# Performance work log

Hardware: AMD Instinct MI355X
Metric: run time of the kernel (lower is better)

## Reference

```python
import jax, jax.numpy as jnp
import numpy as np

N = 50000      # nodes
E = 800000     # edges (before self-loops)
IN_C = 128
H_C = 64
HEADS = 4
OUT_C = 16
NEG_SLOPE = 0.2  # PyG GATConv default


def setup_inputs() -> dict:
    key = jax.random.key(0)
    ks = jax.random.split(key, 11)
    x = jax.random.normal(ks[0], (N, IN_C), dtype=jnp.float32)
    edge_index = jax.random.randint(ks[1], (2, E), 0, N, dtype=jnp.int64)
    def p(k, shape, fan_in):
        return jax.random.normal(k, shape, dtype=jnp.float32) / np.sqrt(fan_in)
    return {
        "x": x,
        "edge_index": edge_index,
        "W1": p(ks[2], (IN_C, HEADS * H_C), IN_C),
        "att_src1": p(ks[3], (HEADS, H_C), H_C),
        "att_dst1": p(ks[4], (HEADS, H_C), H_C),
        "b1": jnp.zeros((HEADS * H_C,), dtype=jnp.float32),
        "W2": p(ks[5], (HEADS * H_C, OUT_C), HEADS * H_C),
        "att_src2": p(ks[6], (1, OUT_C), OUT_C),
        "att_dst2": p(ks[7], (1, OUT_C), OUT_C),
        "b2": jnp.zeros((OUT_C,), dtype=jnp.float32),
    }


def _gat_layer(x, src, dst, W, a_src, a_dst, b, concat):
    n = x.shape[0]
    heads, C = a_src.shape
    h = (x @ W).reshape(n, heads, C)                      # [N,H,C]
    al_s = jnp.einsum('nhc,hc->nh', h, a_src)             # [N,H]
    al_d = jnp.einsum('nhc,hc->nh', h, a_dst)
    e = jax.nn.leaky_relu(al_s[src] + al_d[dst], NEG_SLOPE)  # [E,H]
    # segment softmax over destination neighborhoods
    m = jax.lax.stop_gradient(jax.ops.segment_max(e, dst, num_segments=n))
    p = jnp.exp(e - m[dst])
    denom = jax.ops.segment_sum(p, dst, num_segments=n)
    alpha = p / (denom[dst] + 1e-16)                      # [E,H]
    out = jax.ops.segment_sum(alpha[:, :, None] * h[src], dst, num_segments=n)  # [N,H,C]
    out = out.reshape(n, heads * C) if concat else out.mean(axis=1)
    return out + b


def reference(x, edge_index, W1, att_src1, att_dst1, b1, W2, att_src2, att_dst2, b2):
    # PyG GATConv add_self_loops=True
    loop = jnp.arange(N, dtype=edge_index.dtype)
    src = jnp.concatenate([edge_index[0], loop])
    dst = jnp.concatenate([edge_index[1], loop])
    h = jax.nn.relu(_gat_layer(x, src, dst, W1, att_src1, att_dst1, b1, True))
    out = _gat_layer(h, src, dst, W2, att_src2, att_dst2, b2, False)
    return jax.nn.log_softmax(out, axis=-1)
```

## Files before the change

kernel.cpp:

```cpp
#include <hip/hip_runtime.h>
#include <hip/hip_fp16.h>
#include <cstdint>
#include <cstddef>

#define NEG 0.2f

typedef _Float16 f16x8 __attribute__((ext_vector_type(8)));
typedef float f32x4 __attribute__((ext_vector_type(4)));

__device__ inline float lrelu(float v) { return v > 0.f ? v : NEG * v; }

__global__ void k_swzW(const float* __restrict__ W1, f16x8* __restrict__ W1s) {
  int tau = blockIdx.x * 256 + threadIdx.x;
  if (tau >= 4096) return;
  int l = tau & 63, ct = (tau >> 6) & 15, ks = tau >> 10;
  int col = ct * 16 + (l & 15);
  f16x8 v;
  #pragma unroll
  for (int j = 0; j < 8; j++) {
    int k = ks * 32 + ((j < 4) ? ((l >> 4) * 4 + j) : (16 + (l >> 4) * 4 + (j - 4)));
    v[j] = (_Float16)W1[k * 256 + col];
  }
  W1s[tau] = v;
}

__global__ __launch_bounds__(256) void k_gemm1f(const float* __restrict__ X,
                                                const f16x8* __restrict__ W1s,
                                                const float* __restrict__ as1,
                                                const float* __restrict__ ad1,
                                                __half* __restrict__ H16,
                                                float* __restrict__ als,
                                                float* __restrict__ ald, int N) {
  __shared__ __align__(16) char lds[32768];
  _Float16* A = (_Float16*)lds;
  int t = threadIdx.x;
  int rb = blockIdx.x * 64;
  int l = t & 63, wv = t >> 6;

  #pragma unroll
  for (int i = 0; i < 8; i++) {
    int idx = i * 256 + t;
    int row = idx >> 5, q = idx & 31;
    int gr = rb + row; if (gr >= N) gr = N - 1;
    float4 xv = *(const float4*)(X + (size_t)gr * 128 + q * 4);
    int ks = q >> 3, g = q & 3, hg = (q >> 2) & 1;
    int gran = (ks * 4 + g) ^ (row & 7);
    _Float16* dst = A + row * 128 + gran * 8 + hg * 4;
    dst[0] = (_Float16)xv.x; dst[1] = (_Float16)xv.y;
    dst[2] = (_Float16)xv.z; dst[3] = (_Float16)xv.w;
  }
  __syncthreads();

  f32x4 acc[4][4] = {};
  #pragma unroll
  for (int ks = 0; ks < 4; ks++) {
    f16x8 bfr[4];
    #pragma unroll
    for (int ct = 0; ct < 4; ct++)
      bfr[ct] = W1s[(ks * 16 + wv * 4 + ct) * 64 + l];
    #pragma unroll
    for (int rt = 0; rt < 4; rt++) {
      int row = rt * 16 + (l & 15);
      int gran = (ks * 4 + (l >> 4)) ^ (row & 7);
      f16x8 afr = *(const f16x8*)(A + row * 128 + gran * 8);
      #pragma unroll
      for (int ct = 0; ct < 4; ct++)
        acc[rt][ct] = __builtin_amdgcn_mfma_f32_16x16x32_f16(afr, bfr[ct], acc[rt][ct], 0, 0, 0);
    }
  }

  float asv[4], adv[4];
  #pragma unroll
  for (int ct = 0; ct < 4; ct++) {
    asv[ct] = as1[wv * 64 + ct * 16 + (l & 15)];
    adv[ct] = ad1[wv * 64 + ct * 16 + (l & 15)];
  }
  #pragma unroll
  for (int rt = 0; rt < 4; rt++) {
    #pragma unroll
    for (int j = 0; j < 4; j++) {
      float ps = 0.f, pd = 0.f;
      #pragma unroll
      for (int ct = 0; ct < 4; ct++) {
        ps += acc[rt][ct][j] * asv[ct];
        pd += acc[rt][ct][j] * adv[ct];
      }
      ps += __shfl_xor(ps, 1); ps += __shfl_xor(ps, 2);
      ps += __shfl_xor(ps, 4); ps += __shfl_xor(ps, 8);
      pd += __shfl_xor(pd, 1); pd += __shfl_xor(pd, 2);
      pd += __shfl_xor(pd, 4); pd += __shfl_xor(pd, 8);
      if ((l & 15) == 0) {
        int gr = rb + rt * 16 + (l >> 4) * 4 + j;
        if (gr < N) { als[gr * 4 + wv] = ps; ald[gr * 4 + wv] = pd; }
      }
    }
  }

  __syncthreads();
  _Float16* HL = (_Float16*)lds;
  #pragma unroll
  for (int rt = 0; rt < 4; rt++) {
    #pragma unroll
    for (int j = 0; j < 4; j++) {
      int row = rt * 16 + (l >> 4) * 4 + j;
      #pragma unroll
      for (int ct = 0; ct < 4; ct++) {
        int col = wv * 64 + ct * 16 + (l & 15);
        int g2 = (col >> 3) ^ ((row & 7) << 2);
        HL[row * 256 + g2 * 8 + (col & 7)] = (_Float16)acc[rt][ct][j];
      }
    }
  }
  __syncthreads();
  #pragma unroll
  for (int i = 0; i < 8; i++) {
    int idx = i * 256 + t;
    int row = idx >> 5, g = idx & 31;
    int g2 = g ^ ((row & 7) << 2);
    f32x4 v = *(const f32x4*)(HL + row * 256 + g2 * 8);
    int gr = rb + row;
    if (gr < N) *(f32x4*)((char*)H16 + (size_t)gr * 512 + g * 16) = v;
  }
}

__global__ void k_deg(const int* __restrict__ ei, int* __restrict__ deg, int E, int ET) {
  int e = blockIdx.x * 256 + threadIdx.x;
  if (e >= ET) return;
  int d = (e < E) ? ei[E + e] : e - E;
  atomicAdd(&deg[d], 1);
}

__global__ __launch_bounds__(256) void k_scan_partial(const int* __restrict__ deg,
                                                      int* __restrict__ bsum, int N) {
  __shared__ int sd[256];
  int t = threadIdx.x;
  int base = blockIdx.x * 1024 + t * 4;
  int s = 0;
  #pragma unroll
  for (int j = 0; j < 4; j++) { int i = base + j; s += (i < N) ? deg[i] : 0; }
  sd[t] = s;
  __syncthreads();
  for (int o = 128; o > 0; o >>= 1) {
    if (t < o) sd[t] += sd[t + o];
    __syncthreads();
  }
  if (t == 0) bsum[blockIdx.x] = sd[0];
}

__global__ void k_scan_sums(const int* __restrict__ bsum, int* __restrict__ boff,
                            int* __restrict__ offsets, int NB, int N) {
  if (threadIdx.x == 0 && blockIdx.x == 0) {
    int run = 0;
    for (int i = 0; i < NB; i++) { boff[i] = run; run += bsum[i]; }
    offsets[N] = run;
  }
}

__global__ __launch_bounds__(256) void k_scan_final(const int* __restrict__ deg,
                                                    const int* __restrict__ boff,
                                                    int* __restrict__ offsets,
                                                    int* __restrict__ cursor, int N) {
  __shared__ int sd[256];
  int t = threadIdx.x;
  int base = blockIdx.x * 1024 + t * 4;
  int v[4]; int s = 0;
  #pragma unroll
  for (int j = 0; j < 4; j++) { int i = base + j; v[j] = (i < N) ? deg[i] : 0; s += v[j]; }
  int my = s;
  sd[t] = s;
  __syncthreads();
  for (int o = 1; o < 256; o <<= 1) {
    int add = (t >= o) ? sd[t - o] : 0;
    __syncthreads();
    sd[t] += add;
    __syncthreads();
  }
  int run = sd[t] - my + boff[blockIdx.x];
  #pragma unroll
  for (int j = 0; j < 4; j++) {
    int i = base + j;
    if (i < N) { offsets[i] = run; cursor[i] = run; run += v[j]; }
  }
}

__global__ void k_fill(const int* __restrict__ ei, int* __restrict__ cursor,
                       const float* __restrict__ als, const float* __restrict__ ald,
                       int* __restrict__ csr_src, float* __restrict__ pw1,
                       int* __restrict__ pos_arr, int E, int ET) {
  int e = blockIdx.x * 256 + threadIdx.x;
  if (e >= ET) return;
  int s, d;
  if (e < E) { s = ei[e]; d = ei[E + e]; } else { s = d = e - E; }
  int pos = atomicAdd(&cursor[d], 1);
  csr_src[pos] = s;
  pos_arr[e] = pos;
  float4 a = *(const float4*)(als + (size_t)s * 4);
  float4 b = *(const float4*)(ald + (size_t)d * 4);
  float4 p;
  p.x = __expf(lrelu(a.x + b.x));
  p.y = __expf(lrelu(a.y + b.y));
  p.z = __expf(lrelu(a.z + b.z));
  p.w = __expf(lrelu(a.w + b.w));
  *(float4*)(pw1 + (size_t)pos * 4) = p;
}

__device__ inline void acc8(float4 v, float p, float* a, float& s) {
  __half2 h0 = __builtin_bit_cast(__half2, v.x);
  __half2 h1 = __builtin_bit_cast(__half2, v.y);
  __half2 h2 = __builtin_bit_cast(__half2, v.z);
  __half2 h3 = __builtin_bit_cast(__half2, v.w);
  float2 f0 = __half22float2(h0), f1 = __half22float2(h1);
  float2 f2 = __half22float2(h2), f3 = __half22float2(h3);
  a[0] += p * f0.x; a[1] += p * f0.y; a[2] += p * f1.x; a[3] += p * f1.y;
  a[4] += p * f2.x; a[5] += p * f2.y; a[6] += p * f3.x; a[7] += p * f3.y;
  s += p;
}

__global__ __launch_bounds__(256) void k_agg1(const int* __restrict__ off,
                                              const int* __restrict__ csr_src,
                                              const float* __restrict__ pw1,
                                              const float4* __restrict__ H16,
                                              const float* __restrict__ b1,
                                              __half* __restrict__ H2, int N) {
  int t = threadIdx.x;
  int n = blockIdx.x * 8 + (t >> 5);
  if (n >= N) return;
  int lane = t & 31;
  int g = lane >> 3;
  int st = off[n], en = off[n + 1];
  float a[8] = {0.f, 0.f, 0.f, 0.f, 0.f, 0.f, 0.f, 0.f};
  float s = 0.f;
  int i = st;
  for (; i + 4 <= en; i += 4) {
    int s0 = csr_src[i], s1 = csr_src[i + 1], s2 = csr_src[i + 2], s3 = csr_src[i + 3];
    float p0 = pw1[(size_t)i * 4 + g];
    float p1 = pw1[(size_t)(i + 1) * 4 + g];
    float p2 = pw1[(size_t)(i + 2) * 4 + g];
    float p3 = pw1[(size_t)(i + 3) * 4 + g];
    float4 v0 = H16[(size_t)s0 * 32 + lane];
    float4 v1 = H16[(size_t)s1 * 32 + lane];
    float4 v2 = H16[(size_t)s2 * 32 + lane];
    float4 v3 = H16[(size_t)s3 * 32 + lane];
    acc8(v0, p0, a, s); acc8(v1, p1, a, s); acc8(v2, p2, a, s); acc8(v3, p3, a, s);
  }
  for (; i < en; i++) {
    int s0 = csr_src[i];
    float p0 = pw1[(size_t)i * 4 + g];
    float4 v0 = H16[(size_t)s0 * 32 + lane];
    acc8(v0, p0, a, s);
  }
  float inv = 1.f / (s + 1e-16f);
  int c0 = lane * 8;
  float4 bb0 = *(const float4*)(b1 + c0);
  float4 bb1 = *(const float4*)(b1 + c0 + 4);
  f16x8 o;
  o[0] = (_Float16)fmaxf(a[0] * inv + bb0.x, 0.f);
  o[1] = (_Float16)fmaxf(a[1] * inv + bb0.y, 0.f);
  o[2] = (_Float16)fmaxf(a[2] * inv + bb0.z, 0.f);
  o[3] = (_Float16)fmaxf(a[3] * inv + bb0.w, 0.f);
  o[4] = (_Float16)fmaxf(a[4] * inv + bb1.x, 0.f);
  o[5] = (_Float16)fmaxf(a[5] * inv + bb1.y, 0.f);
  o[6] = (_Float16)fmaxf(a[6] * inv + bb1.z, 0.f);
  o[7] = (_Float16)fmaxf(a[7] * inv + bb1.w, 0.f);
  *(f16x8*)((char*)H2 + (size_t)n * 512 + lane * 16) = o;
}

__global__ __launch_bounds__(256) void k_gemm2(const __half* __restrict__ H2,
                                               const float* __restrict__ W2,
                                               const float* __restrict__ as2,
                                               const float* __restrict__ ad2,
                                               float* __restrict__ Z,
                                               float* __restrict__ als2,
                                               float* __restrict__ ald2, int N) {
  __shared__ float w2s[4096];
  int t = threadIdx.x;
  for (int i = t; i < 4096; i += 256) w2s[i] = W2[i];
  __syncthreads();
  int n = blockIdx.x * 16 + (t >> 4);
  int c = t & 15;
  if (n >= N) return;
  const f16x8* hp = (const f16x8*)((const char*)H2 + (size_t)n * 512);
  float acc = 0.f;
  #pragma unroll 8
  for (int kb = 0; kb < 32; kb++) {
    f16x8 hv = hp[kb];
    #pragma unroll
    for (int j = 0; j < 8; j++)
      acc += (float)hv[j] * w2s[(kb * 8 + j) * 16 + c];
  }
  Z[(size_t)n * 16 + c] = acc;
  float ps = acc * as2[c], pd = acc * ad2[c];
  #pragma unroll
  for (int o = 8; o > 0; o >>= 1) {
    ps += __shfl_down(ps, o, 16);
    pd += __shfl_down(pd, o, 16);
  }
  if (c == 0) { als2[n] = ps; ald2[n] = pd; }
}

__global__ void k_score2p(const int* __restrict__ ei, const int* __restrict__ pos_arr,
                          const float* __restrict__ als2, const float* __restrict__ ald2,
                          float* __restrict__ pw2, int E, int ET) {
  int e = blockIdx.x * 256 + threadIdx.x;
  if (e >= ET) return;
  int s, d;
  if (e < E) { s = ei[e]; d = ei[E + e]; } else { s = d = e - E; }
  float v = lrelu(als2[s] + ald2[d]);
  pw2[pos_arr[e]] = __expf(v);
}

__global__ __launch_bounds__(256) void k_agg2(const int* __restrict__ off,
                                              const int* __restrict__ csr_src,
                                              const float* __restrict__ pw2,
                                              const float* __restrict__ Z,
                                              const float* __restrict__ b2,
                                              float* __restrict__ out, int N) {
  int t = threadIdx.x;
  int n = blockIdx.x * 16 + (t >> 4);
  if (n >= N) return;
  int c = t & 15;
  int st = off[n], en = off[n + 1];
  float s = 0.f, acc = 0.f;
  int i = st;
  for (; i + 4 <= en; i += 4) {
    int s0 = csr_src[i], s1 = csr_src[i + 1], s2 = csr_src[i + 2], s3 = csr_src[i + 3];
    float p0 = pw2[i], p1 = pw2[i + 1], p2 = pw2[i + 2], p3 = pw2[i + 3];
    float z0 = Z[(size_t)s0 * 16 + c];
    float z1 = Z[(size_t)s1 * 16 + c];
    float z2 = Z[(size_t)s2 * 16 + c];
    float z3 = Z[(size_t)s3 * 16 + c];
    acc += p0 * z0 + p1 * z1 + p2 * z2 + p3 * z3;
    s += p0 + p1 + p2 + p3;
  }
  for (; i < en; i++) {
    int s0 = csr_src[i];
    float p0 = pw2[i];
    acc += p0 * Z[(size_t)s0 * 16 + c];
    s += p0;
  }
  float v = acc / (s + 1e-16f) + b2[c];
  float mx = v;
  #pragma unroll
  for (int o = 8; o > 0; o >>= 1) mx = fmaxf(mx, __shfl_xor(mx, o, 16));
  float ex = __expf(v - mx);
  float sm = ex;
  #pragma unroll
  for (int o = 8; o > 0; o >>= 1) sm += __shfl_xor(sm, o, 16);
  out[(size_t)n * 16 + c] = v - mx - logf(sm);
}

extern "C" void kernel_launch(void* const* d_in, const int* in_sizes, int n_in,
                              void* d_out, int out_size, void* d_ws, size_t ws_size,
                              hipStream_t stream) {
  const float* x   = (const float*)d_in[0];
  const int*   ei  = (const int*)d_in[1];
  const float* W1  = (const float*)d_in[2];
  const float* as1 = (const float*)d_in[3];
  const float* ad1 = (const float*)d_in[4];
  const float* b1  = (const float*)d_in[5];
  const float* W2  = (const float*)d_in[6];
  const float* as2 = (const float*)d_in[7];
  const float* ad2 = (const float*)d_in[8];
  const float* b2  = (const float*)d_in[9];
  float* out = (float*)d_out;

  int N  = in_sizes[0] / 128;
  int E  = in_sizes[1] / 2;
  int ET = E + N;
  int NB = (N + 1023) / 1024;

  char* w = (char*)d_ws;
  size_t off_b = 0;
  auto alloc = [&](size_t bytes) -> char* {
    size_t start = (off_b + 255) & ~(size_t)255;
    off_b = start + bytes;
    return w + start;
  };
  __half*   h16  = (__half*)alloc((size_t)N * 256 * 2);
  __half*   h2   = (__half*)alloc((size_t)N * 256 * 2);
  f16x8*    w1s  = (f16x8*)alloc((size_t)4096 * 16);
  float*    als1 = (float*)alloc((size_t)N * 4 * 4);
  float*    ald1 = (float*)alloc((size_t)N * 4 * 4);
  int*      deg  = (int*)alloc((size_t)N * 4);
  int*      offs = (int*)alloc((size_t)(N + 1) * 4);
  int*      cur  = (int*)alloc((size_t)N * 4);
  int*      bsum = (int*)alloc((size_t)NB * 4);
  int*      boff = (int*)alloc((size_t)NB * 4);
  int*      csrs = (int*)alloc((size_t)ET * 4);
  int*      posa = (int*)alloc((size_t)ET * 4);
  float*    pw1  = (float*)alloc((size_t)ET * 4 * 4);
  float*    z    = (float*)alloc((size_t)N * 16 * 4);
  float*    als2 = (float*)alloc((size_t)N * 4);
  float*    ald2 = (float*)alloc((size_t)N * 4);
  float*    pw2  = (float*)alloc((size_t)ET * 4);

  hipMemsetAsync(deg, 0, (size_t)N * 4, stream);

  k_swzW<<<16, 256, 0, stream>>>(W1, w1s);
  k_gemm1f<<<(N + 63) / 64, 256, 0, stream>>>(x, w1s, as1, ad1, h16, als1, ald1, N);
  k_deg<<<(ET + 255) / 256, 256, 0, stream>>>(ei, deg, E, ET);
  k_scan_partial<<<NB, 256, 0, stream>>>(deg, bsum, N);
  k_scan_sums<<<1, 1, 0, stream>>>(bsum, boff, offs, NB, N);
  k_scan_final<<<NB, 256, 0, stream>>>(deg, boff, offs, cur, N);
  k_fill<<<(ET + 255) / 256, 256, 0, stream>>>(ei, cur, als1, ald1, csrs, pw1, posa, E, ET);
  k_agg1<<<(N + 7) / 8, 256, 0, stream>>>(offs, csrs, pw1, (const float4*)h16, b1, h2, N);
  k_gemm2<<<(N + 15) / 16, 256, 0, stream>>>(h2, W2, as2, ad2, z, als2, ald2, N);
  k_score2p<<<(ET + 255) / 256, 256, 0, stream>>>(ei, posa, als2, ald2, pw2, E, ET);
  k_agg2<<<(N + 15) / 16, 256, 0, stream>>>(offs, csrs, pw2, z, b2, out, N);
}
```

Baseline: 249.5 us.

## Fuse layer-1 aggregation with GEMM2 and compute edge scores inline

Removes the precomputed per-edge exp-score arrays (pw1, pw2, pos_arr). The scores are now recomputed on the fly in both aggregation kernels from gathered per-node attention logits. Layer-1 aggregation is fused with the second linear layer and its attention projections: each wavefront-half reduces its own partial Z products by cross-lane shuffles. This drops the H2 intermediate round trip, the k_score2p launch and one kernel launch, at the cost of extra exp work per edge-lane, more shuffles and LDS use in the fused kernel.

```diff
diff --git a/kernel.cpp b/kernel.cpp
--- a/kernel.cpp
+++ b/kernel.cpp
@@ -184,24 +184,13 @@
 }
 
 __global__ void k_fill(const int* __restrict__ ei, int* __restrict__ cursor,
-                       const float* __restrict__ als, const float* __restrict__ ald,
-                       int* __restrict__ csr_src, float* __restrict__ pw1,
-                       int* __restrict__ pos_arr, int E, int ET) {
+                       int* __restrict__ csr_src, int E, int ET) {
   int e = blockIdx.x * 256 + threadIdx.x;
   if (e >= ET) return;
   int s, d;
   if (e < E) { s = ei[e]; d = ei[E + e]; } else { s = d = e - E; }
   int pos = atomicAdd(&cursor[d], 1);
   csr_src[pos] = s;
-  pos_arr[e] = pos;
-  float4 a = *(const float4*)(als + (size_t)s * 4);
-  float4 b = *(const float4*)(ald + (size_t)d * 4);
-  float4 p;
-  p.x = __expf(lrelu(a.x + b.x));
-  p.y = __expf(lrelu(a.y + b.y));
-  p.z = __expf(lrelu(a.z + b.z));
-  p.w = __expf(lrelu(a.w + b.w));
-  *(float4*)(pw1 + (size_t)pos * 4) = p;
 }
 
 __device__ inline void acc8(float4 v, float p, float* a, float& s) {
@@ -216,56 +205,12 @@
   s += p;
 }
 
-__global__ __launch_bounds__(256) void k_agg1(const int* __restrict__ off,
-                                              const int* __restrict__ csr_src,
-                                              const float* __restrict__ pw1,
-                                              const float4* __restrict__ H16,
-                                              const float* __restrict__ b1,
-                                              __half* __restrict__ H2, int N) {
-  int t = threadIdx.x;
-  int n = blockIdx.x * 8 + (t >> 5);
-  if (n >= N) return;
-  int lane = t & 31;
-  int g = lane >> 3;
-  int st = off[n], en = off[n + 1];
-  float a[8] = {0.f, 0.f, 0.f, 0.f, 0.f, 0.f, 0.f, 0.f};
-  float s = 0.f;
-  int i = st;
-  for (; i + 4 <= en; i += 4) {
-    int s0 = csr_src[i], s1 = csr_src[i + 1], s2 = csr_src[i + 2], s3 = csr_src[i + 3];
-    float p0 = pw1[(size_t)i * 4 + g];
-    float p1 = pw1[(size_t)(i + 1) * 4 + g];
-    float p2 = pw1[(size_t)(i + 2) * 4 + g];
-    float p3 = pw1[(size_t)(i + 3) * 4 + g];
-    float4 v0 = H16[(size_t)s0 * 32 + lane];
-    float4 v1 = H16[(size_t)s1 * 32 + lane];
-    float4 v2 = H16[(size_t)s2 * 32 + lane];
-    float4 v3 = H16[(size_t)s3 * 32 + lane];
-    acc8(v0, p0, a, s); acc8(v1, p1, a, s); acc8(v2, p2, a, s); acc8(v3, p3, a, s);
-  }
-  for (; i < en; i++) {
-    int s0 = csr_src[i];
-    float p0 = pw1[(size_t)i * 4 + g];
-    float4 v0 = H16[(size_t)s0 * 32 + lane];
-    acc8(v0, p0, a, s);
-  }
-  float inv = 1.f / (s + 1e-16f);
-  int c0 = lane * 8;
-  float4 bb0 = *(const float4*)(b1 + c0);
-  float4 bb1 = *(const float4*)(b1 + c0 + 4);
-  f16x8 o;
-  o[0] = (_Float16)fmaxf(a[0] * inv + bb0.x, 0.f);
-  o[1] = (_Float16)fmaxf(a[1] * inv + bb0.y, 0.f);
-  o[2] = (_Float16)fmaxf(a[2] * inv + bb0.z, 0.f);
-  o[3] = (_Float16)fmaxf(a[3] * inv + bb0.w, 0.f);
-  o[4] = (_Float16)fmaxf(a[4] * inv + bb1.x, 0.f);
-  o[5] = (_Float16)fmaxf(a[5] * inv + bb1.y, 0.f);
-  o[6] = (_Float16)fmaxf(a[6] * inv + bb1.z, 0.f);
-  o[7] = (_Float16)fmaxf(a[7] * inv + bb1.w, 0.f);
-  *(f16x8*)((char*)H2 + (size_t)n * 512 + lane * 16) = o;
-}
-
-__global__ __launch_bounds__(256) void k_gemm2(const __half* __restrict__ H2,
+__global__ __launch_bounds__(256) void k_agg1x(const int* __restrict__ off,
+                                               const int* __restrict__ csr_src,
+                                               const float* __restrict__ als1,
+                                               const float* __restrict__ ald1,
+                                               const float4* __restrict__ H16,
+                                               const float* __restrict__ b1,
                                                const float* __restrict__ W2,
                                                const float* __restrict__ as2,
                                                const float* __restrict__ ad2,
@@ -276,55 +221,88 @@
   int t = threadIdx.x;
   for (int i = t; i < 4096; i += 256) w2s[i] = W2[i];
   __syncthreads();
-  int n = blockIdx.x * 16 + (t >> 4);
-  int c = t & 15;
+  int n = blockIdx.x * 8 + (t >> 5);
   if (n >= N) return;
-  const f16x8* hp = (const f16x8*)((const char*)H2 + (size_t)n * 512);
-  float acc = 0.f;
-  #pragma unroll 8
-  for (int kb = 0; kb < 32; kb++) {
-    f16x8 hv = hp[kb];
+  int lane = t & 31;
+  int g = lane >> 3;
+  float aldn = ald1[n * 4 + g];
+  int st = off[n], en = off[n + 1];
+  float a[8] = {0.f, 0.f, 0.f, 0.f, 0.f, 0.f, 0.f, 0.f};
+  float s = 0.f;
+  int i = st;
+  for (; i + 4 <= en; i += 4) {
+    int s0 = csr_src[i], s1 = csr_src[i + 1], s2 = csr_src[i + 2], s3 = csr_src[i + 3];
+    float p0 = __expf(lrelu(als1[s0 * 4 + g] + aldn));
+    float p1 = __expf(lrelu(als1[s1 * 4 + g] + aldn));
+    float p2 = __expf(lrelu(als1[s2 * 4 + g] + aldn));
+    float p3 = __expf(lrelu(als1[s3 * 4 + g] + aldn));
+    float4 v0 = H16[(size_t)s0 * 32 + lane];
+    float4 v1 = H16[(size_t)s1 * 32 + lane];
+    float4 v2 = H16[(size_t)s2 * 32 + lane];
+    float4 v3 = H16[(size_t)s3 * 32 + lane];
+    acc8(v0, p0, a, s); acc8(v1, p1, a, s); acc8(v2, p2, a, s); acc8(v3, p3, a, s);
+  }
+  for (; i < en; i++) {
+    int s0 = csr_src[i];
+    float p0 = __expf(lrelu(als1[s0 * 4 + g] + aldn));
+    float4 v0 = H16[(size_t)s0 * 32 + lane];
+    acc8(v0, p0, a, s);
+  }
+  float inv = 1.f / (s + 1e-16f);
+  int c0 = lane * 8;
+  float h2v[8];
+  #pragma unroll
+  for (int j = 0; j < 8; j++)
+    h2v[j] = fmaxf(a[j] * inv + b1[c0 + j], 0.f);
+  float zp[16];
+  #pragma unroll
+  for (int c = 0; c < 16; c++) {
+    float acc2 = 0.f;
     #pragma unroll
     for (int j = 0; j < 8; j++)
-      acc += (float)hv[j] * w2s[(kb * 8 + j) * 16 + c];
-  }
-  Z[(size_t)n * 16 + c] = acc;
-  float ps = acc * as2[c], pd = acc * ad2[c];
-  #pragma unroll
-  for (int o = 8; o > 0; o >>= 1) {
-    ps += __shfl_down(ps, o, 16);
-    pd += __shfl_down(pd, o, 16);
-  }
-  if (c == 0) { als2[n] = ps; ald2[n] = pd; }
-}
-
-__global__ void k_score2p(const int* __restrict__ ei, const int* __restrict__ pos_arr,
-                          const float* __restrict__ als2, const float* __restrict__ ald2,
-                          float* __restrict__ pw2, int E, int ET) {
-  int e = blockIdx.x * 256 + threadIdx.x;
-  if (e >= ET) return;
-  int s, d;
-  if (e < E) { s = ei[e]; d = ei[E + e]; } else { s = d = e - E; }
-  float v = lrelu(als2[s] + ald2[d]);
-  pw2[pos_arr[e]] = __expf(v);
-}
-
-__global__ __launch_bounds__(256) void k_agg2(const int* __restrict__ off,
-                                              const int* __restrict__ csr_src,
-                                              const float* __restrict__ pw2,
-                                              const float* __restrict__ Z,
-                                              const float* __restrict__ b2,
-                                              float* __restrict__ out, int N) {
+      acc2 += h2v[j] * w2s[(c0 + j) * 16 + c];
+    zp[c] = acc2;
+  }
+  #pragma unroll
+  for (int m = 1; m <= 16; m <<= 1) {
+    #pragma unroll
+    for (int c = 0; c < 16; c++)
+      zp[c] += __shfl_xor(zp[c], m);
+  }
+  if (lane < 16) {
+    float zc = zp[lane];
+    Z[(size_t)n * 16 + lane] = zc;
+    float ps = zc * as2[lane], pd = zc * ad2[lane];
+    #pragma unroll
+    for (int o = 8; o > 0; o >>= 1) {
+      ps += __shfl_down(ps, o, 16);
+      pd += __shfl_down(pd, o, 16);
+    }
+    if (lane == 0) { als2[n] = ps; ald2[n] = pd; }
+  }
+}
+
+__global__ __launch_bounds__(256) void k_agg2x(const int* __restrict__ off,
+                                               const int* __restrict__ csr_src,
+                                               const float* __restrict__ als2,
+                                               const float* __restrict__ ald2,
+                                               const float* __restrict__ Z,
+                                               const float* __restrict__ b2,
+                                               float* __restrict__ out, int N) {
   int t = threadIdx.x;
   int n = blockIdx.x * 16 + (t >> 4);
   if (n >= N) return;
   int c = t & 15;
+  float aldn = ald2[n];
   int st = off[n], en = off[n + 1];
   float s = 0.f, acc = 0.f;
   int i = st;
   for (; i + 4 <= en; i += 4) {
     int s0 = csr_src[i], s1 = csr_src[i + 1], s2 = csr_src[i + 2], s3 = csr_src[i + 3];
-    float p0 = pw2[i], p1 = pw2[i + 1], p2 = pw2[i + 2], p3 = pw2[i + 3];
+    float p0 = __expf(lrelu(als2[s0] + aldn));
+    float p1 = __expf(lrelu(als2[s1] + aldn));
+    float p2 = __expf(lrelu(als2[s2] + aldn));
+    float p3 = __expf(lrelu(als2[s3] + aldn));
     float z0 = Z[(size_t)s0 * 16 + c];
     float z1 = Z[(size_t)s1 * 16 + c];
     float z2 = Z[(size_t)s2 * 16 + c];
@@ -334,7 +312,7 @@
   }
   for (; i < en; i++) {
     int s0 = csr_src[i];
-    float p0 = pw2[i];
+    float p0 = __expf(lrelu(als2[s0] + aldn));
     acc += p0 * Z[(size_t)s0 * 16 + c];
     s += p0;
   }
@@ -377,7 +355,6 @@
     return w + start;
   };
   __half*   h16  = (__half*)alloc((size_t)N * 256 * 2);
-  __half*   h2   = (__half*)alloc((size_t)N * 256 * 2);
   f16x8*    w1s  = (f16x8*)alloc((size_t)4096 * 16);
   float*    als1 = (float*)alloc((size_t)N * 4 * 4);
   float*    ald1 = (float*)alloc((size_t)N * 4 * 4);
@@ -387,12 +364,9 @@
   int*      bsum = (int*)alloc((size_t)NB * 4);
   int*      boff = (int*)alloc((size_t)NB * 4);
   int*      csrs = (int*)alloc((size_t)ET * 4);
-  int*      posa = (int*)alloc((size_t)ET * 4);
-  float*    pw1  = (float*)alloc((size_t)ET * 4 * 4);
   float*    z    = (float*)alloc((size_t)N * 16 * 4);
   float*    als2 = (float*)alloc((size_t)N * 4);
   float*    ald2 = (float*)alloc((size_t)N * 4);
-  float*    pw2  = (float*)alloc((size_t)ET * 4);
 
   hipMemsetAsync(deg, 0, (size_t)N * 4, stream);
 
@@ -402,9 +376,8 @@
   k_scan_partial<<<NB, 256, 0, stream>>>(deg, bsum, N);
   k_scan_sums<<<1, 1, 0, stream>>>(bsum, boff, offs, NB, N);
   k_scan_final<<<NB, 256, 0, stream>>>(deg, boff, offs, cur, N);
-  k_fill<<<(ET + 255) / 256, 256, 0, stream>>>(ei, cur, als1, ald1, csrs, pw1, posa, E, ET);
-  k_agg1<<<(N + 7) / 8, 256, 0, stream>>>(offs, csrs, pw1, (const float4*)h16, b1, h2, N);
-  k_gemm2<<<(N + 15) / 16, 256, 0, stream>>>(h2, W2, as2, ad2, z, als2, ald2, N);
-  k_score2p<<<(ET + 255) / 256, 256, 0, stream>>>(ei, posa, als2, ald2, pw2, E, ET);
-  k_agg2<<<(N + 15) / 16, 256, 0, stream>>>(offs, csrs, pw2, z, b2, out, N);
-}
+  k_fill<<<(ET + 255) / 256, 256, 0, stream>>>(ei, cur, csrs, E, ET);
+  k_agg1x<<<(N + 7) / 8, 256, 0, stream>>>(offs, csrs, als1, ald1, (const float4*)h16,
+                                           b1, W2, as2, ad2, z, als2, ald2, N);
+  k_agg2x<<<(N + 15) / 16, 256, 0, stream>>>(offs, csrs, als2, ald2, z, b2, out, N);
+}
```

Result: slower. 285.8 us (+14.5%).
